# Kernel optimization log

Measured on AMD Instinct MI355X. Metric: run time of the kernel, lower is better.

## Reference

```python
import jax, jax.numpy as jnp
import numpy as np

TAU = 1.0  # temperature of the NeuralSort relaxation


def _neural_sort(s, tau=TAU):
    """NeuralSort soft permutation matrix for scores s of shape (n,).
    Returns (n, n) row-stochastic matrix; row i ~ one-hot of i-th largest score."""
    n = s.shape[0]
    A_sum = jnp.abs(s[:, None] - s[None, :]).sum(-1)              # (n,)
    scaling = (n + 1 - 2 * jnp.arange(1, n + 1)).astype(s.dtype)  # (n,)
    scores = (scaling[:, None] * s[None, :] - A_sum[None, :]) / tau
    return jax.nn.softmax(scores, axis=-1)


def _soft_perm_gt(events, d):
    """Vectorized version of _get_soft_perm.
    events: (n,) int {0,1}; d: (n,) float durations. Returns (n, n) float32."""
    n = events.shape[0]
    idx = jnp.argsort(d)                 # ascending durations
    e_s = events[idx]                    # events in sorted order
    c = jnp.cumsum(e_s) - e_s            # exclusive event count before position i
    i = jnp.arange(n)
    lo = c                               # first allowed rank column
    hi = jnp.where(e_s == 1, i + 1, n)   # one past last allowed rank column
    j = jnp.arange(n)
    mask = (j[None, :] >= lo[:, None]) & (j[None, :] < hi[:, None])
    rows = mask.astype(jnp.float32) / (hi - lo)[:, None].astype(jnp.float32)
    inv = jnp.argsort(idx)               # perm_un_ascending @ M == rows re-indexed
    return rows[inv]


def _bce(p, y):
    # torch BCELoss: clamp log terms at -100, mean over all elements
    logp = jnp.maximum(jnp.log(p), -100.0)
    log1mp = jnp.maximum(jnp.log1p(-p), -100.0)
    return -(y * logp + (1.0 - y) * log1mp).mean()


def setup_inputs() -> dict:
    key = jax.random.key(0)
    k1, k2, k3 = jax.random.split(key, 3)
    n, C = 2048, 8
    logits = jax.random.normal(k1, (n, C), dtype=jnp.float32)
    durations = jax.random.uniform(k2, (n, C), dtype=jnp.float32)
    events = jax.random.randint(k3, (n, C), 0, 2).astype(jnp.int32)
    return {"logits": logits, "events": events, "durations": durations}


def reference(logits, events, durations):
    def col_loss(lh, e, d):
        p = _neural_sort(lh)        # (n, n) soft permutation prediction
        y = _soft_perm_gt(e, d)     # (n, n) soft permutation label
        return _bce(p, y)

    losses = jax.vmap(col_loss, in_axes=(1, 1, 1))(logits, events, durations)  # (C,)
    m = losses > 0
    denom = jnp.maximum(jnp.sum(m), 1).astype(losses.dtype)
    return jnp.sum(jnp.where(m, losses, 0.0)) / denom
```

## Files before the change

### kernel.cpp

```cpp
#include <hip/hip_runtime.h>
#include <hip/hip_bf16.h>
#include <math.h>

#define N 2048
#define NC 8


#if __has_builtin(__builtin_amdgcn_exp2f)
__device__ __forceinline__ float fexp2(float x) { return __builtin_amdgcn_exp2f(x); }
#else
__device__ __forceinline__ float fexp2(float x) { return exp2f(x); }
#endif
#if __has_builtin(__builtin_amdgcn_logf)
__device__ __forceinline__ float flog2(float x) { return __builtin_amdgcn_logf(x); }
#else
__device__ __forceinline__ float flog2(float x) { return log2f(x); }
#endif

#define INV_LN2 1.4426950408889634f
#define LN2_D   0.6931471805599453
#define CLAMP2  (-144.26950408889634f)

__global__ __launch_bounds__(256) void k_prep(const float* __restrict__ logits,
                                              const float* __restrict__ dur,
                                              const int* __restrict__ ev,
                                              float2* __restrict__ pack,
                                              int* __restrict__ lohi,
                                              double* __restrict__ acc,
                                              unsigned* __restrict__ counter) {
    __shared__ float s[N];
    __shared__ double part[256];
    __shared__ unsigned long long keys[N];
    __shared__ int pr[256], pv[256];

    int b = blockIdx.x;
    int tid = threadIdx.x;

    if (b == 0) {
        if (tid < 8) acc[tid] = 0.0;
        else if (tid == 8) counter[0] = 0u;
    }

    if (b < 256) {
        int col = b >> 5, chunk = b & 31;
        for (int k = 0; k < N / 256; ++k) {
            int i = tid + k * 256;
            s[i] = logits[i * NC + col];
        }
        __syncthreads();
        int jl = tid & 63, slice = tid >> 6;
        int j = chunk * 64 + jl;
        float sj = s[j];
        int base = slice * 512;
        double a0 = 0.0, a1 = 0.0, a2 = 0.0, a3 = 0.0;
        #pragma unroll 2
        for (int i = 0; i < 512; i += 4) {
            a0 += (double)fabsf(sj - s[base + i]);
            a1 += (double)fabsf(sj - s[base + i + 1]);
            a2 += (double)fabsf(sj - s[base + i + 2]);
            a3 += (double)fabsf(sj - s[base + i + 3]);
        }
        part[tid] = (a0 + a1) + (a2 + a3);
        __syncthreads();
        if (tid < 64) {
            double v = ((part[tid] + part[tid + 64]) + part[tid + 128]) + part[tid + 192];
            pack[col * N + j] = make_float2(sj * INV_LN2, (float)v * INV_LN2);
        }
    } else {
        int b2 = b - 256;
        int col = b2 >> 5, chunk = b2 & 31;
        for (int k = 0; k < N / 256; ++k) {
            int i = tid + k * 256;
            unsigned int db = __float_as_uint(dur[i * NC + col]);
            int e = ev[i * NC + col];
            keys[i] = ((unsigned long long)db << 32) | (unsigned int)((i << 1) | e);
        }
        __syncthreads();
        int jl = tid & 63, slice = tid >> 6;
        int j = chunk * 64 + jl;
        unsigned long long kj = keys[j];
        int base = slice * 512;
        int rank = 0, evlt = 0;
        #pragma unroll 4
        for (int i = 0; i < 512; ++i) {
            unsigned long long ki = keys[base + i];
            int lt = (ki < kj) ? 1 : 0;
            rank += lt;
            evlt += lt & (int)(ki & 1ull);
        }
        pr[tid] = rank;
        pv[tid] = evlt;
        __syncthreads();
        if (tid < 64) {
            int r = ((pr[tid] + pr[tid + 64]) + pr[tid + 128]) + pr[tid + 192];
            int v = ((pv[tid] + pv[tid + 64]) + pv[tid + 128]) + pv[tid + 192];
            int e = (int)(kj & 1ull);
            int hi = e ? (r + 1) : N;
            lohi[col * N + j] = v | (hi << 16);
        }
    }
}

__global__ __launch_bounds__(256) void k_bce(const float2* __restrict__ pack,
                                             const int* __restrict__ lohi,
                                             double* __restrict__ acc,
                                             unsigned* __restrict__ counter,
                                             float* __restrict__ out) {
    int col = blockIdx.x >> 7;
    int rg  = blockIdx.x & 127;
    __shared__ float4 sa4[N / 2];
    __shared__ double bsum[4];
    int tid = threadIdx.x;
    int wave = tid >> 6, lane = tid & 63;

    const float4* p4 = (const float4*)(pack + (size_t)col * N);
    #pragma unroll
    for (int k = 0; k < 4; ++k) {
        int i = tid + (k << 8);
        sa4[i] = p4[i];
    }
    __syncthreads();

    int row0 = (rg << 4) + (wave << 2);
    float sc0 = (float)(N - 1 - 2 * row0);

    int lh[4];
    #pragma unroll
    for (int c = 0; c < 4; ++c) lh[c] = lohi[col * N + row0 + c];

    float m = -INFINITY;
    #pragma unroll
    for (int k = 0; k < 16; ++k) {
        float4 q = sa4[lane + (k << 6)];
        float t0 = fmaf(sc0, q.x, -q.y);
        float t1 = fmaf(sc0, q.z, -q.w);
        m = fmaxf(m, fmaxf(t0, t1));
    }
    #pragma unroll
    for (int off = 32; off > 0; off >>= 1)
        m = fmaxf(m, __shfl_xor(m, off, 64));

    float se0 = 0.0f, se1 = 0.0f, se2 = 0.0f, se3 = 0.0f;
    #pragma unroll
    for (int k = 0; k < 16; ++k) {
        float4 q = sa4[lane + (k << 6)];
        {
            float g = fexp2(-(q.x + q.x));
            float E = fexp2(fmaf(sc0, q.x, -q.y) - m);
            se0 += E; E *= g;
            se1 += E; E *= g;
            se2 += E; E *= g;
            se3 += E;
        }
        {
            float g = fexp2(-(q.z + q.z));
            float E = fexp2(fmaf(sc0, q.z, -q.w) - m);
            se0 += E; E *= g;
            se1 += E; E *= g;
            se2 += E; E *= g;
            se3 += E;
        }
    }
    #pragma unroll
    for (int off = 32; off > 0; off >>= 1) {
        se0 += __shfl_xor(se0, off, 64);
        se1 += __shfl_xor(se1, off, 64);
        se2 += __shfl_xor(se2, off, 64);
        se3 += __shfl_xor(se3, off, 64);
    }
    float se[4] = {se0, se1, se2, se3};

    float C2v[4], yv[4];
    unsigned lo[4], wl[4];
    double rbase = 0.0;
    #pragma unroll
    for (int c = 0; c < 4; ++c) {
        float L2 = flog2(se[c]);
        rbase -= 2048.0 * (double)L2;
        C2v[c] = CLAMP2 + L2;
        lo[c] = (unsigned)(lh[c] & 0xffff);
        wl[c] = (unsigned)((lh[c] >> 16) & 0xffff) - lo[c];
        yv[c] = 1.0f / (float)wl[c];
    }

    float a1[4] = {0.0f, 0.0f, 0.0f, 0.0f};
    float a2[4] = {0.0f, 0.0f, 0.0f, 0.0f};
    #pragma unroll
    for (int k = 0; k < 16; ++k) {
        float4 q = sa4[lane + (k << 6)];
        int j0 = (lane + (k << 6)) << 1;
        {
            float tsv = q.x + q.x;
            float g = fexp2(-tsv);
            float x = fmaf(sc0, q.x, -q.y) - m;
            float E = fexp2(x);
            #pragma unroll
            for (int c = 0; c < 4; ++c) {
                float mx2 = fmaxf(flog2(se[c] - E), C2v[c]);
                a1[c] += mx2;
                float mx1 = fmaxf(x, C2v[c]);
                float w = ((unsigned)(j0 - lo[c]) < wl[c]) ? (mx1 - mx2) : 0.0f;
                a2[c] += w;
                E *= g;
                x -= tsv;
            }
        }
        {
            float tsv = q.z + q.z;
            float g = fexp2(-tsv);
            float x = fmaf(sc0, q.z, -q.w) - m;
            float E = fexp2(x);
            #pragma unroll
            for (int c = 0; c < 4; ++c) {
                float mx2 = fmaxf(flog2(se[c] - E), C2v[c]);
                a1[c] += mx2;
                float mx1 = fmaxf(x, C2v[c]);
                float w = ((unsigned)(j0 + 1 - lo[c]) < wl[c]) ? (mx1 - mx2) : 0.0f;
                a2[c] += w;
                E *= g;
                x -= tsv;
            }
        }
    }
    float r = 0.0f;
    #pragma unroll
    for (int c = 0; c < 4; ++c) r += fmaf(yv[c], a2[c], a1[c]);
    #pragma unroll
    for (int off = 32; off > 0; off >>= 1)
        r += __shfl_xor(r, off, 64);

    if (lane == 0) bsum[wave] = rbase + (double)r;
    __syncthreads();
    if (tid == 0) {
        double tot = (bsum[0] + bsum[1]) + (bsum[2] + bsum[3]);
        atomicAdd(&acc[col], LN2_D * tot);
        __threadfence();
        unsigned old = atomicAdd(counter, 1u);
        if (old == (unsigned)(NC * 128 - 1)) {
            __threadfence();
            float ssum = 0.0f;
            int cnt = 0;
            for (int c = 0; c < NC; ++c) {
                double av2 = atomicAdd(&acc[c], 0.0);
                float lc = (float)(-av2 / ((double)N * (double)N));
                if (lc > 0.0f) { ssum += lc; cnt++; }
            }
            out[0] = ssum / (float)(cnt > 0 ? cnt : 1);
        }
    }
}

extern "C" void kernel_launch(void* const* d_in, const int* in_sizes, int n_in,
                              void* d_out, int out_size, void* d_ws, size_t ws_size,
                              hipStream_t stream) {
    const float* logits    = (const float*)d_in[0];
    const int*   events    = (const int*)d_in[1];
    const float* durations = (const float*)d_in[2];
    float* out = (float*)d_out;

    char* ws = (char*)d_ws;
    double*   acc     = (double*)ws;
    float2*   pack    = (float2*)(ws + 64);
    int*      lohi    = (int*)(ws + 64 + (size_t)NC * N * sizeof(float2));
    unsigned* counter = (unsigned*)(ws + 64 + (size_t)NC * N * (sizeof(float2) + sizeof(int)));

    k_prep<<<dim3(512), 256, 0, stream>>>(logits, durations, events, pack, lohi, acc, counter);
    k_bce<<<dim3(NC * 128), 256, 0, stream>>>(pack, lohi, acc, counter, out);
}
```

Measured before the change: 102.3 us.

## Compute pairwise abs-diff sums via rank, sorted prefix sums instead of O(n^2) doubles

Replaces the O(n^2) double-precision sum of |s_j - s_i| with a closed form. Each logit's rank comes from a 64-bit key comparison count, and a new per-column kernel scatters the values into sorted order and takes a prefix scan. Rank-based formula A = s*(2r-n) + T - 2*prefix[r] then yields the same sums. This removes heavy FP64 work but adds a third kernel launch and an 8-block serial scan stage.

```diff
diff --git a/kernel.cpp b/kernel.cpp
--- a/kernel.cpp
+++ b/kernel.cpp
@@ -24,12 +24,10 @@
 __global__ __launch_bounds__(256) void k_prep(const float* __restrict__ logits,
                                               const float* __restrict__ dur,
                                               const int* __restrict__ ev,
-                                              float2* __restrict__ pack,
+                                              int* __restrict__ rankbuf,
                                               int* __restrict__ lohi,
                                               double* __restrict__ acc,
                                               unsigned* __restrict__ counter) {
-    __shared__ float s[N];
-    __shared__ double part[256];
     __shared__ unsigned long long keys[N];
     __shared__ int pr[256], pv[256];
 
@@ -45,26 +43,28 @@
         int col = b >> 5, chunk = b & 31;
         for (int k = 0; k < N / 256; ++k) {
             int i = tid + k * 256;
-            s[i] = logits[i * NC + col];
+            unsigned bb = __float_as_uint(logits[i * NC + col]);
+            unsigned ou = (bb & 0x80000000u) ? ~bb : (bb | 0x80000000u);
+            keys[i] = ((unsigned long long)ou << 32) | (unsigned)i;
         }
         __syncthreads();
         int jl = tid & 63, slice = tid >> 6;
         int j = chunk * 64 + jl;
-        float sj = s[j];
+        unsigned long long kj = keys[j];
         int base = slice * 512;
-        double a0 = 0.0, a1 = 0.0, a2 = 0.0, a3 = 0.0;
-        #pragma unroll 2
+        int r0 = 0, r1 = 0, r2 = 0, r3 = 0;
+        #pragma unroll 4
         for (int i = 0; i < 512; i += 4) {
-            a0 += (double)fabsf(sj - s[base + i]);
-            a1 += (double)fabsf(sj - s[base + i + 1]);
-            a2 += (double)fabsf(sj - s[base + i + 2]);
-            a3 += (double)fabsf(sj - s[base + i + 3]);
-        }
-        part[tid] = (a0 + a1) + (a2 + a3);
+            r0 += (keys[base + i]     < kj);
+            r1 += (keys[base + i + 1] < kj);
+            r2 += (keys[base + i + 2] < kj);
+            r3 += (keys[base + i + 3] < kj);
+        }
+        pr[tid] = (r0 + r1) + (r2 + r3);
         __syncthreads();
         if (tid < 64) {
-            double v = ((part[tid] + part[tid + 64]) + part[tid + 128]) + part[tid + 192];
-            pack[col * N + j] = make_float2(sj * INV_LN2, (float)v * INV_LN2);
+            int r = ((pr[tid] + pr[tid + 64]) + pr[tid + 128]) + pr[tid + 192];
+            rankbuf[col * N + j] = r;
         }
     } else {
         int b2 = b - 256;
@@ -98,6 +98,62 @@
             int hi = e ? (r + 1) : N;
             lohi[col * N + j] = v | (hi << 16);
         }
+    }
+}
+
+__global__ __launch_bounds__(256) void k_scanpack(const float* __restrict__ logits,
+                                                  const int* __restrict__ rankbuf,
+                                                  float2* __restrict__ pack) {
+    int col = blockIdx.x;
+    __shared__ float  ssort[N];
+    __shared__ double pex[N];
+    __shared__ double wsum[4];
+    int tid = threadIdx.x;
+    int lane = tid & 63, wave = tid >> 6;
+
+    float sv[8];
+    int   rv[8];
+    #pragma unroll
+    for (int k = 0; k < 8; ++k) {
+        int j = tid + (k << 8);
+        sv[k] = logits[j * NC + col];
+        rv[k] = rankbuf[col * N + j];
+        ssort[rv[k]] = sv[k];
+    }
+    __syncthreads();
+
+    double loc[8];
+    double c = 0.0;
+    #pragma unroll
+    for (int k = 0; k < 8; ++k) {
+        loc[k] = c;
+        c += (double)ssort[tid * 8 + k];
+    }
+    double inc = c;
+    #pragma unroll
+    for (int off = 1; off < 64; off <<= 1) {
+        double y = __shfl_up(inc, off, 64);
+        if (lane >= off) inc += y;
+    }
+    if (lane == 63) wsum[wave] = inc;
+    __syncthreads();
+    double woff = 0.0;
+    #pragma unroll
+    for (int w = 0; w < 4; ++w)
+        if (w < wave) woff += wsum[w];
+    double T = ((wsum[0] + wsum[1]) + (wsum[2] + wsum[3]));
+    double exc = woff + (inc - c);
+    #pragma unroll
+    for (int k = 0; k < 8; ++k) pex[tid * 8 + k] = exc + loc[k];
+    __syncthreads();
+
+    #pragma unroll
+    for (int k = 0; k < 8; ++k) {
+        int j = tid + (k << 8);
+        float s = sv[k];
+        int   r = rv[k];
+        double A = (double)s * (double)(2 * r - N) + T - 2.0 * pex[r];
+        pack[col * N + j] = make_float2(s * INV_LN2, (float)A * INV_LN2);
     }
 }
 
@@ -263,7 +319,9 @@
     float2*   pack    = (float2*)(ws + 64);
     int*      lohi    = (int*)(ws + 64 + (size_t)NC * N * sizeof(float2));
     unsigned* counter = (unsigned*)(ws + 64 + (size_t)NC * N * (sizeof(float2) + sizeof(int)));
-
-    k_prep<<<dim3(512), 256, 0, stream>>>(logits, durations, events, pack, lohi, acc, counter);
+    int*      rankbuf = (int*)(ws + 64 + (size_t)NC * N * (sizeof(float2) + sizeof(int)) + 64);
+
+    k_prep<<<dim3(512), 256, 0, stream>>>(logits, durations, events, rankbuf, lohi, acc, counter);
+    k_scanpack<<<dim3(NC), 256, 0, stream>>>(logits, rankbuf, pack);
     k_bce<<<dim3(NC * 128), 256, 0, stream>>>(pack, lohi, acc, counter, out);
 }
```

After: 107.9 us. +5.4%, slower.
